# Optimization experiments

Hardware: AMD Instinct MI355X
Metric: run time of the kernel (lower is better)

Reference implementation:

```python
import jax, jax.numpy as jnp
import numpy as np

B, D, K, V, T = 128, 1280, 49, 10000, 40  # batch, hidden, spatial keys, vocab, max words
SOS = 0


def setup_inputs() -> dict:
    key = jax.random.key(0)
    ks = jax.random.split(key, 20)
    s = 0.02
    inp = {
        "img_channels": jax.random.normal(ks[0], (B, D, 7, 7), jnp.float32),
        "pooled": jax.random.normal(ks[1], (B, D), jnp.float32),
        # LSTM (torch order i,f,g,o), stored as [in, 4*hidden]
        "W_ih": jax.random.normal(ks[2], (D, 4 * D), jnp.float32) * s,
        "W_hh": jax.random.normal(ks[3], (D, 4 * D), jnp.float32) * s,
        "b_ih": jnp.zeros((4 * D,), jnp.float32),
        "b_hh": jnp.zeros((4 * D,), jnp.float32),
        # cross-attention: fc_q on hidden (D->D), fc_k/fc_v on spatial (K->K)
        "Wq": jax.random.normal(ks[4], (D, D), jnp.float32) * s,
        "bq": jnp.zeros((D,), jnp.float32),
        "Wk": jax.random.normal(ks[5], (K, K), jnp.float32) * s,
        "bk": jnp.zeros((K,), jnp.float32),
        "Wv": jax.random.normal(ks[6], (K, K), jnp.float32) * s,
        "bv": jnp.zeros((K,), jnp.float32),
        # gating linears (2D -> D)
        "Wh": jax.random.normal(ks[7], (2 * D, D), jnp.float32) * s,
        "bh": jnp.zeros((D,), jnp.float32),
        "Wc": jax.random.normal(ks[8], (2 * D, D), jnp.float32) * s,
        "bc": jnp.zeros((D,), jnp.float32),
        # vocab projection and embedding
        "Wp": jax.random.normal(ks[9], (D, V), jnp.float32) * s,
        "bp": jnp.zeros((V,), jnp.float32),
        "embed": jax.random.normal(ks[10], (V, D), jnp.float32) * s,
    }
    return inp


def _cross_attn(ch, h, Wq, bq, Wk, bk, Wv, bv):
    # ch: [B, D, K]   h: [B, D]
    q = jnp.tanh(h @ Wq + bq)                      # [B, D]
    k = jnp.tanh(ch @ Wk + bk)                     # [B, D, K]
    scores = jnp.einsum('bdk,bd->bk', k, q) / 7.0  # [B, K]
    w = jax.nn.softmax(scores, axis=1)
    v = jnp.tanh(ch @ Wv + bv)                     # [B, D, K]
    return jnp.einsum('bk,bdk->bd', w, v)          # [B, D]


def reference(img_channels, pooled, W_ih, W_hh, b_ih, b_hh,
              Wq, bq, Wk, bk, Wv, bv, Wh, bh, Wc, bc, Wp, bp, embed):
    ch = img_channels.reshape(B, D, K)

    def lstm_cell(x, h, c):
        g = x @ W_ih + b_ih + h @ W_hh + b_hh      # [B, 4D]
        i, f, gg, o = jnp.split(g, 4, axis=-1)
        c_new = jax.nn.sigmoid(f) * c + jax.nn.sigmoid(i) * jnp.tanh(gg)
        h_new = jax.nn.sigmoid(o) * jnp.tanh(c_new)
        return h_new, c_new

    x0 = jnp.broadcast_to(embed[SOS], (B, D))      # start token embedding

    def step(carry, _):
        x, h, c = carry
        h_new, c_new = lstm_cell(x, h, c)
        out = h_new                                # LSTM output, seq_len=1
        # greedy next-token feed (no teacher forcing)
        idx = jnp.argmax(out @ Wp + bp, axis=-1)   # [B]
        x_next = embed[idx]                        # [B, D]
        # attention-gated state update
        ha = _cross_attn(ch, h_new, Wq, bq, Wk, bk, Wv, bv)
        ca = _cross_attn(ch, c_new, Wq, bq, Wk, bk, Wv, bv)
        h2 = jnp.tanh(jnp.concatenate([ha, h_new], -1) @ Wh + bh)
        c2 = jnp.tanh(jnp.concatenate([ca, c_new], -1) @ Wc + bc)
        return (x_next, h2, c2), out

    _, outs = jax.lax.scan(step, (x0, pooled, pooled), None, length=T - 1)
    pred = jnp.concatenate([x0[None], outs], axis=0)   # [T, B, D]
    res = jnp.einsum('tbd,dn->bnt', pred, Wp) + bp[None, :, None]  # [B, V, T]
    return res
```

## Files before the change

kernel.cpp:

```cpp
#include <hip/hip_runtime.h>
#include <hip/hip_fp16.h>

#define NB 128
#define ND 1280
#define NK 49
#define NV 10000
#define NT 40
#define N4D 5120

typedef unsigned long long u64;

__device__ __forceinline__ void gemm_core(
    const float* __restrict__ A0, const float* __restrict__ A1, int asplit, int lda,
    const float* __restrict__ B0, const float* __restrict__ B1, int bsplit, int ldb,
    int n0, int N, int kbase, int kc, float* __restrict__ C)
{
  __shared__ float Al[2][16][132];
  __shared__ float Bl[2][16][68];
  const int tid = threadIdx.x;
  const int tn = tid & 15, tm = tid >> 4;
  float acc[8][4];
#pragma unroll
  for (int i = 0; i < 8; ++i)
#pragma unroll
    for (int j = 0; j < 4; ++j) acc[i][j] = 0.f;

  const int am  = tid >> 1;
  const int ac0 = (tid & 1) * 8;
  const int br  = tid >> 4;
  const int bc  = (tid & 15) * 4;
  const int bcol = n0 + bc;
  const int ntile = kc >> 4;

  float4 ra0, ra1, rb;

  auto load_tile = [&](int t) {
    const int kg = kbase + (t << 4);
    const float* Ab = (kg < asplit) ? (A0 + kg) : (A1 + (kg - asplit));
    const float* Bb = (kg < bsplit) ? (B0 + (size_t)kg * ldb)
                                    : (B1 + (size_t)(kg - bsplit) * ldb);
    ra0 = *(const float4*)(Ab + (size_t)am * lda + ac0);
    ra1 = *(const float4*)(Ab + (size_t)am * lda + ac0 + 4);
    if (bcol < N) rb = *(const float4*)(Bb + (size_t)br * ldb + bcol);
    else rb = make_float4(0.f, 0.f, 0.f, 0.f);
  };
  auto store_tile = [&](int buf) {
    Al[buf][ac0 + 0][am] = ra0.x; Al[buf][ac0 + 1][am] = ra0.y;
    Al[buf][ac0 + 2][am] = ra0.z; Al[buf][ac0 + 3][am] = ra0.w;
    Al[buf][ac0 + 4][am] = ra1.x; Al[buf][ac0 + 5][am] = ra1.y;
    Al[buf][ac0 + 6][am] = ra1.z; Al[buf][ac0 + 7][am] = ra1.w;
    *(float4*)&Bl[buf][br][bc] = rb;
  };

  load_tile(0); store_tile(0); __syncthreads();
  for (int t = 0; t < ntile; ++t) {
    if (t + 1 < ntile) load_tile(t + 1);
    const int buf = t & 1;
#pragma unroll
    for (int kk = 0; kk < 16; ++kk) {
      const float4 a0 = *(const float4*)&Al[buf][kk][tm * 8];
      const float4 a1 = *(const float4*)&Al[buf][kk][tm * 8 + 4];
      const float4 b4 = *(const float4*)&Bl[buf][kk][tn * 4];
      const float amv[8] = {a0.x, a0.y, a0.z, a0.w, a1.x, a1.y, a1.z, a1.w};
      const float bvv[4] = {b4.x, b4.y, b4.z, b4.w};
#pragma unroll
      for (int i = 0; i < 8; ++i)
#pragma unroll
        for (int j = 0; j < 4; ++j)
          acc[i][j] = fmaf(amv[i], bvv[j], acc[i][j]);
    }
    __syncthreads();
    if (t + 1 < ntile) { store_tile((t + 1) & 1); __syncthreads(); }
  }
  const int ccol = n0 + tn * 4;
  if (ccol < N) {
#pragma unroll
    for (int i = 0; i < 8; ++i) {
      float4 v = make_float4(acc[i][0], acc[i][1], acc[i][2], acc[i][3]);
      *(float4*)(C + (size_t)(tm * 8 + i) * N + ccol) = v;
    }
  }
}

__global__ __launch_bounds__(256) void k_gates(const float* __restrict__ x,
    const float* __restrict__ h, const float* __restrict__ Wih,
    const float* __restrict__ Whh, float* __restrict__ part)
{
  int n0 = blockIdx.x * 64, s = blockIdx.y;
  gemm_core(x, h, ND, ND, Wih, Whh, ND, N4D, n0, N4D, s * 320, 320,
            part + (size_t)s * NB * N4D);
}
__global__ __launch_bounds__(256) void k_logits(const float* __restrict__ hn,
    const float* __restrict__ Wp, float* __restrict__ part)
{
  int n0 = blockIdx.x * 64, s = blockIdx.y;
  gemm_core(hn, hn, 1 << 28, ND, Wp, Wp, 1 << 28, NV, n0, NV, s * 320, 320,
            part + (size_t)s * NB * NV);
}
__global__ __launch_bounds__(256) void k_qgemm(const float* __restrict__ hn,
    const float* __restrict__ cn, const float* __restrict__ Wq, float* __restrict__ part)
{
  int n0 = blockIdx.x * 64, s = blockIdx.y, z = blockIdx.z;
  const float* A = z ? cn : hn;
  gemm_core(A, A, 1 << 28, ND, Wq, Wq, 1 << 28, ND, n0, ND, s * 320, 320,
            part + (size_t)s * 256 * ND + (size_t)z * NB * ND);
}
__global__ __launch_bounds__(256) void k_ggemm(const float* __restrict__ att,
    const float* __restrict__ hn, const float* __restrict__ cn,
    const float* __restrict__ Wh, const float* __restrict__ Wc, float* __restrict__ part)
{
  int n0 = blockIdx.x * 64, s = blockIdx.y, z = blockIdx.z;
  const float* A0 = att + (size_t)z * NB * ND;
  const float* A1 = z ? cn : hn;
  const float* Bw = z ? Wc : Wh;
  gemm_core(A0, A1, ND, ND, Bw, Bw, 1 << 28, ND, n0, ND, s * 320, 320,
            part + (size_t)z * 8 * NB * ND + (size_t)s * NB * ND);
}

__global__ __launch_bounds__(256) void k_lstm(const float* __restrict__ part,
    const float* __restrict__ bih, const float* __restrict__ bhh,
    const float* __restrict__ c_st, float* __restrict__ hn, float* __restrict__ cn,
    u64* __restrict__ amax)
{
  int idx = blockIdx.x * 256 + threadIdx.x;
  if (idx < NB) amax[idx] = 0ULL;
  int b = idx / ND, d = idx % ND;
  const float* gp = part + (size_t)b * N4D;
  float gi = bih[d]          + bhh[d];
  float gf = bih[ND + d]     + bhh[ND + d];
  float gg = bih[2 * ND + d] + bhh[2 * ND + d];
  float go = bih[3 * ND + d] + bhh[3 * ND + d];
#pragma unroll
  for (int s = 0; s < 8; ++s) {
    const float* p = gp + (size_t)s * NB * N4D;
    gi += p[d]; gf += p[ND + d]; gg += p[2 * ND + d]; go += p[3 * ND + d];
  }
  float c = c_st[idx];
  float si = 1.f / (1.f + expf(-gi));
  float sf = 1.f / (1.f + expf(-gf));
  float so = 1.f / (1.f + expf(-go));
  float cnew = sf * c + si * tanhf(gg);
  float hnew = so * tanhf(cnew);
  cn[idx] = cnew; hn[idx] = hnew;
}

__device__ __forceinline__ u64 pack_max(float v, int n) {
  unsigned u = __float_as_uint(v);
  u = (u & 0x80000000u) ? ~u : (u | 0x80000000u);
  return ((u64)u << 32) | (u64)(0xFFFFFFFFu - (unsigned)n);
}
__global__ __launch_bounds__(256) void k_lred(const float* __restrict__ part,
    const float* __restrict__ bp, __half* __restrict__ stage, float* __restrict__ outp,
    int tslice, int staged, u64* __restrict__ amax)
{
  int b = blockIdx.y;
  int nbeg = blockIdx.x * 2000, nend = nbeg + 2000;
  u64 best = 0ULL;
  for (int n = nbeg + (int)threadIdx.x; n < nend; n += 256) {
    float v = bp[n];
#pragma unroll
    for (int s = 0; s < 4; ++s) v += part[(size_t)s * NB * NV + (size_t)b * NV + n];
    if (staged) stage[(size_t)tslice * NB * NV + (size_t)b * NV + n] = __float2half(v);
    else outp[((size_t)b * NV + n) * NT + tslice] = v;
    u64 p = pack_max(v, n);
    best = best > p ? best : p;
  }
  __shared__ u64 red[256];
  red[threadIdx.x] = best; __syncthreads();
  for (int off = 128; off > 0; off >>= 1) {
    if ((int)threadIdx.x < off) {
      u64 o = red[threadIdx.x + off];
      if (o > red[threadIdx.x]) red[threadIdx.x] = o;
    }
    __syncthreads();
  }
  if (threadIdx.x == 0) atomicMax(amax + b, red[0]);
}

__global__ __launch_bounds__(256) void k_attn(const float* __restrict__ qpart,
    const float* __restrict__ bq, const float* __restrict__ kmatT,
    const float* __restrict__ vmat, float* __restrict__ att,
    const u64* __restrict__ amax, const float* __restrict__ embed,
    float* __restrict__ x_st)
{
  int bb = blockIdx.x;
  if (bb >= NB) {
    int half = bb - NB;
    for (int idx = half * 81920 + (int)threadIdx.x; idx < (half + 1) * 81920; idx += 256) {
      int b = idx / ND, d = idx % ND;
      int n = (int)(0xFFFFFFFFu - (unsigned)(amax[b] & 0xFFFFFFFFULL));
      x_st[idx] = embed[(size_t)n * ND + d];
    }
    return;
  }
  __shared__ float qh[ND], qc[ND];
  __shared__ float sc[2][64];
  __shared__ float wl[2][64];
  int tid = threadIdx.x;
  for (int d = tid; d < ND; d += 256) {
    float ah = bq[d], ac = bq[d];
#pragma unroll
    for (int s = 0; s < 4; ++s) {
      ah += qpart[(size_t)s * 256 * ND + (size_t)bb * ND + d];
      ac += qpart[(size_t)s * 256 * ND + (size_t)(NB + bb) * ND + d];
    }
    qh[d] = tanhf(ah); qc[d] = tanhf(ac);
  }
  __syncthreads();
  int w = tid >> 6, lane = tid & 63;
  for (int kk = w; kk < NK; kk += 4) {
    const float4* kr = (const float4*)(kmatT + ((size_t)bb * NK + kk) * ND);
    float ah = 0.f, ac = 0.f;
#pragma unroll
    for (int c = 0; c < 5; ++c) {
      float4 kv = kr[c * 64 + lane];
      const float4 q4h = *(const float4*)&qh[(c * 64 + lane) * 4];
      const float4 q4c = *(const float4*)&qc[(c * 64 + lane) * 4];
      ah += kv.x * q4h.x + kv.y * q4h.y + kv.z * q4h.z + kv.w * q4h.w;
      ac += kv.x * q4c.x + kv.y * q4c.y + kv.z * q4c.z + kv.w * q4c.w;
    }
#pragma unroll
    for (int off = 32; off > 0; off >>= 1) {
      ah += __shfl_down(ah, off);
      ac += __shfl_down(ac, off);
    }
    if (lane == 0) { sc[0][kk] = ah / 7.0f; sc[1][kk] = ac / 7.0f; }
  }
  __syncthreads();
  if (w < 2) {
    float s = (lane < NK) ? sc[w][lane] : -3.4e38f;
    float mx = s;
#pragma unroll
    for (int off = 32; off > 0; off >>= 1) mx = fmaxf(mx, __shfl_xor(mx, off));
    float e = (lane < NK) ? expf(s - mx) : 0.f;
    float sum = e;
#pragma unroll
    for (int off = 32; off > 0; off >>= 1) sum += __shfl_xor(sum, off);
    wl[w][lane] = (lane < NK) ? e / sum : 0.f;
  }
  __syncthreads();
  for (int d = tid; d < ND; d += 256) {
    const float4* vr = (const float4*)(vmat + ((size_t)bb * ND + d) * 52);
    float ah = 0.f, ac = 0.f;
#pragma unroll
    for (int c4 = 0; c4 < 13; ++c4) {
      float4 v = vr[c4];
      ah += wl[0][c4 * 4 + 0] * v.x + wl[0][c4 * 4 + 1] * v.y
          + wl[0][c4 * 4 + 2] * v.z + wl[0][c4 * 4 + 3] * v.w;
      ac += wl[1][c4 * 4 + 0] * v.x + wl[1][c4 * 4 + 1] * v.y
          + wl[1][c4 * 4 + 2] * v.z + wl[1][c4 * 4 + 3] * v.w;
    }
    att[(size_t)bb * ND + d] = ah;
    att[(size_t)(NB + bb) * ND + d] = ac;
  }
}

__global__ __launch_bounds__(256) void k_gred(const float* __restrict__ part,
    const float* __restrict__ bh, const float* __restrict__ bc,
    float* __restrict__ h_st, float* __restrict__ c_st)
{
  int idx = blockIdx.x * 256 + threadIdx.x;
  int z = idx / (NB * ND); int rem = idx - z * NB * ND; int d = rem % ND;
  float v = z ? bc[d] : bh[d];
  const float* p = part + (size_t)z * 8 * NB * ND + rem;
#pragma unroll
  for (int s = 0; s < 8; ++s) v += p[(size_t)s * NB * ND];
  v = tanhf(v);
  if (z) c_st[rem] = v; else h_st[rem] = v;
}

__global__ __launch_bounds__(256) void k_init(const float* __restrict__ pooled,
    const float* __restrict__ embed, float* __restrict__ h, float* __restrict__ c,
    float* __restrict__ x)
{
  int idx = blockIdx.x * 256 + threadIdx.x;
  float p = pooled[idx];
  h[idx] = p; c[idx] = p;
  x[idx] = embed[idx % ND];
}

__global__ __launch_bounds__(256) void k_kv(const float* __restrict__ ch,
    const float* __restrict__ Wk, const float* __restrict__ bk,
    const float* __restrict__ Wv, const float* __restrict__ bv,
    float* __restrict__ kmatT, float* __restrict__ vmat)
{
  __shared__ float sbuf[256 * NK];
  __shared__ float Wkl[NK * NK], Wvl[NK * NK], bkl[64], bvl[64];
  int b = blockIdx.y, d0 = blockIdx.x * 256, tid = threadIdx.x;
  for (int i = tid; i < NK * NK; i += 256) { Wkl[i] = Wk[i]; Wvl[i] = Wv[i]; }
  if (tid < NK) { bkl[tid] = bk[tid]; bvl[tid] = bv[tid]; }
  const size_t chbase = ((size_t)b * ND + d0) * NK;
  for (int i = tid; i < 256 * NK; i += 256) sbuf[i] = ch[chbase + i];
  __syncthreads();
  float rr[NK];
#pragma unroll
  for (int k = 0; k < NK; ++k) rr[k] = sbuf[tid * NK + k];
  size_t vb = ((size_t)b * ND + d0 + tid) * 52;
  for (int j = 0; j < NK; ++j) {
    float a = bvl[j];
#pragma unroll
    for (int k = 0; k < NK; ++k) a = fmaf(rr[k], Wvl[k * NK + j], a);
    vmat[vb + j] = tanhf(a);
  }
  vmat[vb + 49] = 0.f; vmat[vb + 50] = 0.f; vmat[vb + 51] = 0.f;
  __syncthreads();
  for (int j = 0; j < NK; ++j) {
    float a = bkl[j];
#pragma unroll
    for (int k = 0; k < NK; ++k) a = fmaf(rr[k], Wkl[k * NK + j], a);
    sbuf[j * 256 + tid] = tanhf(a);
  }
  __syncthreads();
  for (int i = tid; i < NK * 256; i += 256) {
    int j = i >> 8, dd = i & 255;
    kmatT[((size_t)b * NK + j) * ND + d0 + dd] = sbuf[i];
  }
}

__global__ __launch_bounds__(256) void k_l0(const float* __restrict__ embed,
    const float* __restrict__ Wp, const float* __restrict__ bp,
    __half* __restrict__ stage, float* __restrict__ outp, int staged)
{
  __shared__ float e0[ND];
  int tid = threadIdx.x;
  for (int i = tid; i < ND; i += 256) e0[i] = embed[i];
  __syncthreads();
  int n = blockIdx.x * 256 + tid;
  if (n >= NV) return;
  float a = bp[n];
  for (int d = 0; d < ND; ++d) a = fmaf(e0[d], Wp[(size_t)d * NV + n], a);
  if (staged) {
    for (int b = 0; b < NB; ++b) stage[(size_t)b * NV + n] = __float2half(a);
  } else {
    for (int b = 0; b < NB; ++b) outp[((size_t)b * NV + n) * NT] = a;
  }
}

__global__ __launch_bounds__(256) void k_tr(const __half* __restrict__ stage,
    float* __restrict__ outp)
{
  __shared__ float tl[64][41];
  int b = blockIdx.y, n0 = blockIdx.x * 64, tid = threadIdx.x;
  for (int i = tid; i < 2560; i += 256) {
    int t = i >> 6, n = i & 63;
    float v = (n0 + n < NV)
        ? __half2float(stage[(size_t)t * NB * NV + (size_t)b * NV + n0 + n]) : 0.f;
    tl[n][t] = v;
  }
  __syncthreads();
  for (int i = tid; i < 640; i += 256) {
    int row = i / 10, c4 = i % 10;
    if (n0 + row < NV) {
      float4 v = make_float4(tl[row][c4 * 4], tl[row][c4 * 4 + 1],
                             tl[row][c4 * 4 + 2], tl[row][c4 * 4 + 3]);
      *(float4*)(outp + ((size_t)b * NV + n0 + row) * NT + c4 * 4) = v;
    }
  }
}

extern "C" void kernel_launch(void* const* d_in, const int* in_sizes, int n_in,
                              void* d_out, int out_size, void* d_ws, size_t ws_size,
                              hipStream_t stream) {
  const float* ch     = (const float*)d_in[0];
  const float* pooled = (const float*)d_in[1];
  const float* Wih    = (const float*)d_in[2];
  const float* Whh    = (const float*)d_in[3];
  const float* bih    = (const float*)d_in[4];
  const float* bhh    = (const float*)d_in[5];
  const float* Wq     = (const float*)d_in[6];
  const float* bq     = (const float*)d_in[7];
  const float* Wk     = (const float*)d_in[8];
  const float* bk     = (const float*)d_in[9];
  const float* Wv     = (const float*)d_in[10];
  const float* bv     = (const float*)d_in[11];
  const float* Wh     = (const float*)d_in[12];
  const float* bh     = (const float*)d_in[13];
  const float* Wc     = (const float*)d_in[14];
  const float* bc     = (const float*)d_in[15];
  const float* Wp     = (const float*)d_in[16];
  const float* bp     = (const float*)d_in[17];
  const float* embed  = (const float*)d_in[18];
  float* outp = (float*)d_out;

  char* w = (char*)d_ws;
  size_t off = 0;
  auto alloc = [&](size_t bytes) {
    void* p = w + off; off += (bytes + 255) & ~(size_t)255; return p;
  };
  float* kmatT  = (float*)alloc((size_t)NB * NK * ND * 4);
  float* vmat   = (float*)alloc((size_t)NB * ND * 52 * 4);
  float* h_st   = (float*)alloc((size_t)NB * ND * 4);
  float* c_st   = (float*)alloc((size_t)NB * ND * 4);
  float* x_st   = (float*)alloc((size_t)NB * ND * 4);
  float* h_new  = (float*)alloc((size_t)NB * ND * 4);
  float* c_new  = (float*)alloc((size_t)NB * ND * 4);
  float* gpart  = (float*)alloc((size_t)8 * NB * N4D * 4);
  float* lpart  = (float*)alloc((size_t)4 * NB * NV * 4);
  float* qpart  = (float*)alloc((size_t)4 * 256 * ND * 4);
  float* attb   = (float*)alloc((size_t)256 * ND * 4);
  float* g2part = (float*)alloc((size_t)2 * 8 * NB * ND * 4);
  u64*   amax   = (u64*)alloc((size_t)NB * 8);
  __half* stage = (__half*)alloc((size_t)NT * NB * NV * 2);
  int staged = (ws_size >= off) ? 1 : 0;

  k_init<<<640, 256, 0, stream>>>(pooled, embed, h_st, c_st, x_st);
  k_kv<<<dim3(5, NB), 256, 0, stream>>>(ch, Wk, bk, Wv, bv, kmatT, vmat);
  k_l0<<<40, 256, 0, stream>>>(embed, Wp, bp, stage, outp, staged);

  for (int s = 0; s < NT - 1; ++s) {
    k_gates<<<dim3(80, 8), 256, 0, stream>>>(x_st, h_st, Wih, Whh, gpart);
    k_lstm<<<640, 256, 0, stream>>>(gpart, bih, bhh, c_st, h_new, c_new, amax);
    k_logits<<<dim3(157, 4), 256, 0, stream>>>(h_new, Wp, lpart);
    k_lred<<<dim3(5, NB), 256, 0, stream>>>(lpart, bp, stage, outp, s + 1, staged, amax);
    k_qgemm<<<dim3(20, 4, 2), 256, 0, stream>>>(h_new, c_new, Wq, qpart);
    k_attn<<<130, 256, 0, stream>>>(qpart, bq, kmatT, vmat, attb, amax, embed, x_st);
    k_ggemm<<<dim3(20, 8, 2), 256, 0, stream>>>(attb, h_new, c_new, Wh, Wc, g2part);
    k_gred<<<1280, 256, 0, stream>>>(g2part, bh, bc, h_st, c_st);
  }
  if (staged) k_tr<<<dim3(157, NB), 256, 0, stream>>>(stage, outp);
}
```

Measured before the change: 16.63 ms.

## Fuse per-step kernels into persistent cooperative kernel with grid syncs

Replaces eight kernel launches per decode step with one persistent cooperative kernel of 512 blocks that runs the seven phases and separates them with grid-wide barriers. It also changes the split-K partitioning (6, 3, 6 and 12 splits) so each phase fills the fixed grid, and runs the logit reduction concurrently with the Wq GEMM in one phase. The aim is to remove launch overhead and idle tails between many small kernels. In exchange it depends on 512 blocks being co-resident (two per CU), and falls back to per-phase launches if the cooperative launch fails.

```diff
diff --git a/kernel.cpp b/kernel.cpp
--- a/kernel.cpp
+++ b/kernel.cpp
@@ -1,5 +1,8 @@
 #include <hip/hip_runtime.h>
 #include <hip/hip_fp16.h>
+#include <hip/hip_cooperative_groups.h>
+
+namespace cg = cooperative_groups;
 
 #define NB 128
 #define ND 1280
@@ -7,8 +10,20 @@
 #define NV 10000
 #define NT 40
 #define N4D 5120
+#define GRID 512
 
 typedef unsigned long long u64;
+
+struct P {
+  const float *ch, *pooled, *Wih, *Whh, *bih, *bhh, *Wq, *bq, *Wk, *bk, *Wv, *bv,
+              *Wh, *bh, *Wc, *bc, *Wp, *bp, *embed;
+  float *outp;
+  float *kmatT, *vmat, *h_st, *c_st, *x_st, *h_new, *c_new,
+        *gpart, *lpart, *qpart, *attb, *g2part;
+  u64 *amax;
+  __half *stage;
+  int staged;
+};
 
 __device__ __forceinline__ void gemm_core(
     const float* __restrict__ A0, const float* __restrict__ A1, int asplit, int lda,
@@ -82,134 +97,75 @@
   }
 }
 
-__global__ __launch_bounds__(256) void k_gates(const float* __restrict__ x,
-    const float* __restrict__ h, const float* __restrict__ Wih,
-    const float* __restrict__ Whh, float* __restrict__ part)
-{
-  int n0 = blockIdx.x * 64, s = blockIdx.y;
-  gemm_core(x, h, ND, ND, Wih, Whh, ND, N4D, n0, N4D, s * 320, 320,
-            part + (size_t)s * NB * N4D);
-}
-__global__ __launch_bounds__(256) void k_logits(const float* __restrict__ hn,
-    const float* __restrict__ Wp, float* __restrict__ part)
-{
-  int n0 = blockIdx.x * 64, s = blockIdx.y;
-  gemm_core(hn, hn, 1 << 28, ND, Wp, Wp, 1 << 28, NV, n0, NV, s * 320, 320,
-            part + (size_t)s * NB * NV);
-}
-__global__ __launch_bounds__(256) void k_qgemm(const float* __restrict__ hn,
-    const float* __restrict__ cn, const float* __restrict__ Wq, float* __restrict__ part)
-{
-  int n0 = blockIdx.x * 64, s = blockIdx.y, z = blockIdx.z;
-  const float* A = z ? cn : hn;
-  gemm_core(A, A, 1 << 28, ND, Wq, Wq, 1 << 28, ND, n0, ND, s * 320, 320,
-            part + (size_t)s * 256 * ND + (size_t)z * NB * ND);
-}
-__global__ __launch_bounds__(256) void k_ggemm(const float* __restrict__ att,
-    const float* __restrict__ hn, const float* __restrict__ cn,
-    const float* __restrict__ Wh, const float* __restrict__ Wc, float* __restrict__ part)
-{
-  int n0 = blockIdx.x * 64, s = blockIdx.y, z = blockIdx.z;
-  const float* A0 = att + (size_t)z * NB * ND;
-  const float* A1 = z ? cn : hn;
-  const float* Bw = z ? Wc : Wh;
-  gemm_core(A0, A1, ND, ND, Bw, Bw, 1 << 28, ND, n0, ND, s * 320, 320,
-            part + (size_t)z * 8 * NB * ND + (size_t)s * NB * ND);
-}
-
-__global__ __launch_bounds__(256) void k_lstm(const float* __restrict__ part,
-    const float* __restrict__ bih, const float* __restrict__ bhh,
-    const float* __restrict__ c_st, float* __restrict__ hn, float* __restrict__ cn,
-    u64* __restrict__ amax)
-{
-  int idx = blockIdx.x * 256 + threadIdx.x;
-  if (idx < NB) amax[idx] = 0ULL;
-  int b = idx / ND, d = idx % ND;
-  const float* gp = part + (size_t)b * N4D;
-  float gi = bih[d]          + bhh[d];
-  float gf = bih[ND + d]     + bhh[ND + d];
-  float gg = bih[2 * ND + d] + bhh[2 * ND + d];
-  float go = bih[3 * ND + d] + bhh[3 * ND + d];
-#pragma unroll
-  for (int s = 0; s < 8; ++s) {
-    const float* p = gp + (size_t)s * NB * N4D;
-    gi += p[d]; gf += p[ND + d]; gg += p[2 * ND + d]; go += p[3 * ND + d];
-  }
-  float c = c_st[idx];
-  float si = 1.f / (1.f + expf(-gi));
-  float sf = 1.f / (1.f + expf(-gf));
-  float so = 1.f / (1.f + expf(-go));
-  float cnew = sf * c + si * tanhf(gg);
-  float hnew = so * tanhf(cnew);
-  cn[idx] = cnew; hn[idx] = hnew;
-}
-
 __device__ __forceinline__ u64 pack_max(float v, int n) {
   unsigned u = __float_as_uint(v);
   u = (u & 0x80000000u) ? ~u : (u | 0x80000000u);
   return ((u64)u << 32) | (u64)(0xFFFFFFFFu - (unsigned)n);
 }
-__global__ __launch_bounds__(256) void k_lred(const float* __restrict__ part,
-    const float* __restrict__ bp, __half* __restrict__ stage, float* __restrict__ outp,
-    int tslice, int staged, u64* __restrict__ amax)
-{
-  int b = blockIdx.y;
-  int nbeg = blockIdx.x * 2000, nend = nbeg + 2000;
+
+__device__ void ph_lstm(int blk, const P& p) {
+  int tid = threadIdx.x;
+  for (int idx = blk * 256 + tid; idx < NB * ND; idx += GRID * 256) {
+    if (idx < NB) p.amax[idx] = 0ULL;
+    int b = idx / ND, d = idx % ND;
+    const float* gp = p.gpart + (size_t)b * N4D;
+    float gi = p.bih[d]          + p.bhh[d];
+    float gf = p.bih[ND + d]     + p.bhh[ND + d];
+    float gg = p.bih[2 * ND + d] + p.bhh[2 * ND + d];
+    float go = p.bih[3 * ND + d] + p.bhh[3 * ND + d];
+#pragma unroll
+    for (int s = 0; s < 6; ++s) {
+      const float* q = gp + (size_t)s * NB * N4D;
+      gi += q[d]; gf += q[ND + d]; gg += q[2 * ND + d]; go += q[3 * ND + d];
+    }
+    float c = p.c_st[idx];
+    float si = 1.f / (1.f + expf(-gi));
+    float sf = 1.f / (1.f + expf(-gf));
+    float so = 1.f / (1.f + expf(-go));
+    float cnew = sf * c + si * tanhf(gg);
+    p.c_new[idx] = cnew; p.h_new[idx] = so * tanhf(cnew);
+  }
+}
+
+__device__ void ph_lred(int b, int nbeg, int step, const P& p) {
+  __shared__ u64 red[256];
+  int tid = threadIdx.x;
   u64 best = 0ULL;
-  for (int n = nbeg + (int)threadIdx.x; n < nend; n += 256) {
-    float v = bp[n];
-#pragma unroll
-    for (int s = 0; s < 4; ++s) v += part[(size_t)s * NB * NV + (size_t)b * NV + n];
-    if (staged) stage[(size_t)tslice * NB * NV + (size_t)b * NV + n] = __float2half(v);
-    else outp[((size_t)b * NV + n) * NT + tslice] = v;
-    u64 p = pack_max(v, n);
-    best = best > p ? best : p;
-  }
-  __shared__ u64 red[256];
-  red[threadIdx.x] = best; __syncthreads();
+  for (int n = nbeg + tid; n < nbeg + 5000; n += 256) {
+    float v = p.bp[n];
+#pragma unroll
+    for (int s = 0; s < 3; ++s) v += p.lpart[(size_t)s * NB * NV + (size_t)b * NV + n];
+    if (p.staged) p.stage[(size_t)(step + 1) * NB * NV + (size_t)b * NV + n] = __float2half(v);
+    else p.outp[((size_t)b * NV + n) * NT + step + 1] = v;
+    u64 q = pack_max(v, n);
+    best = best > q ? best : q;
+  }
+  red[tid] = best; __syncthreads();
   for (int off = 128; off > 0; off >>= 1) {
-    if ((int)threadIdx.x < off) {
-      u64 o = red[threadIdx.x + off];
-      if (o > red[threadIdx.x]) red[threadIdx.x] = o;
-    }
+    if (tid < off) { u64 o = red[tid + off]; if (o > red[tid]) red[tid] = o; }
     __syncthreads();
   }
-  if (threadIdx.x == 0) atomicMax(amax + b, red[0]);
-}
-
-__global__ __launch_bounds__(256) void k_attn(const float* __restrict__ qpart,
-    const float* __restrict__ bq, const float* __restrict__ kmatT,
-    const float* __restrict__ vmat, float* __restrict__ att,
-    const u64* __restrict__ amax, const float* __restrict__ embed,
-    float* __restrict__ x_st)
-{
-  int bb = blockIdx.x;
-  if (bb >= NB) {
-    int half = bb - NB;
-    for (int idx = half * 81920 + (int)threadIdx.x; idx < (half + 1) * 81920; idx += 256) {
-      int b = idx / ND, d = idx % ND;
-      int n = (int)(0xFFFFFFFFu - (unsigned)(amax[b] & 0xFFFFFFFFULL));
-      x_st[idx] = embed[(size_t)n * ND + d];
-    }
-    return;
-  }
+  if (tid == 0) atomicMax(p.amax + b, red[0]);
+}
+
+__device__ void ph_attn(int bb, const P& p) {
   __shared__ float qh[ND], qc[ND];
   __shared__ float sc[2][64];
   __shared__ float wl[2][64];
   int tid = threadIdx.x;
   for (int d = tid; d < ND; d += 256) {
-    float ah = bq[d], ac = bq[d];
-#pragma unroll
-    for (int s = 0; s < 4; ++s) {
-      ah += qpart[(size_t)s * 256 * ND + (size_t)bb * ND + d];
-      ac += qpart[(size_t)s * 256 * ND + (size_t)(NB + bb) * ND + d];
+    float ah = p.bq[d], ac = p.bq[d];
+#pragma unroll
+    for (int s = 0; s < 6; ++s) {
+      ah += p.qpart[(size_t)s * 256 * ND + (size_t)bb * ND + d];
+      ac += p.qpart[(size_t)s * 256 * ND + (size_t)(NB + bb) * ND + d];
     }
     qh[d] = tanhf(ah); qc[d] = tanhf(ac);
   }
   __syncthreads();
   int w = tid >> 6, lane = tid & 63;
   for (int kk = w; kk < NK; kk += 4) {
-    const float4* kr = (const float4*)(kmatT + ((size_t)bb * NK + kk) * ND);
+    const float4* kr = (const float4*)(p.kmatT + ((size_t)bb * NK + kk) * ND);
     float ah = 0.f, ac = 0.f;
 #pragma unroll
     for (int c = 0; c < 5; ++c) {
@@ -240,7 +196,7 @@
   }
   __syncthreads();
   for (int d = tid; d < ND; d += 256) {
-    const float4* vr = (const float4*)(vmat + ((size_t)bb * ND + d) * 52);
+    const float4* vr = (const float4*)(p.vmat + ((size_t)bb * ND + d) * 52);
     float ah = 0.f, ac = 0.f;
 #pragma unroll
     for (int c4 = 0; c4 < 13; ++c4) {
@@ -250,23 +206,97 @@
       ac += wl[1][c4 * 4 + 0] * v.x + wl[1][c4 * 4 + 1] * v.y
           + wl[1][c4 * 4 + 2] * v.z + wl[1][c4 * 4 + 3] * v.w;
     }
-    att[(size_t)bb * ND + d] = ah;
-    att[(size_t)(NB + bb) * ND + d] = ac;
-  }
-}
-
-__global__ __launch_bounds__(256) void k_gred(const float* __restrict__ part,
-    const float* __restrict__ bh, const float* __restrict__ bc,
-    float* __restrict__ h_st, float* __restrict__ c_st)
-{
-  int idx = blockIdx.x * 256 + threadIdx.x;
-  int z = idx / (NB * ND); int rem = idx - z * NB * ND; int d = rem % ND;
-  float v = z ? bc[d] : bh[d];
-  const float* p = part + (size_t)z * 8 * NB * ND + rem;
-#pragma unroll
-  for (int s = 0; s < 8; ++s) v += p[(size_t)s * NB * ND];
-  v = tanhf(v);
-  if (z) c_st[rem] = v; else h_st[rem] = v;
+    p.attb[(size_t)bb * ND + d] = ah;
+    p.attb[(size_t)(NB + bb) * ND + d] = ac;
+  }
+}
+
+__device__ void do_phase(int phase, int blk, int step, const P& p) {
+  const int tid = threadIdx.x;
+  switch (phase) {
+    case 1:
+      if (blk < 480) {
+        int tile = blk / 6, sk = blk % 6;
+        int kbase = sk * 432, kc = (sk == 5) ? 400 : 432;
+        gemm_core(p.x_st, p.h_st, ND, ND, p.Wih, p.Whh, ND, N4D,
+                  tile * 64, N4D, kbase, kc, p.gpart + (size_t)sk * NB * N4D);
+      }
+      break;
+    case 2: ph_lstm(blk, p); break;
+    case 3:
+      if (blk < 471) {
+        int tile = blk / 3, sk = blk % 3;
+        int kbase = sk * 432, kc = (sk == 2) ? 416 : 432;
+        gemm_core(p.h_new, p.h_new, 1 << 28, ND, p.Wp, p.Wp, 1 << 28, NV,
+                  tile * 64, NV, kbase, kc, p.lpart + (size_t)sk * NB * NV);
+      }
+      break;
+    case 4:
+      if (blk < 256) ph_lred(blk >> 1, (blk & 1) * 5000, step, p);
+      else if (blk >= 272) {
+        int q = blk - 272, z = q / 120, r = q % 120;
+        int tile = r / 6, sk = r % 6;
+        int kbase = sk * 224, kc = (sk == 5) ? 160 : 224;
+        const float* A = z ? p.c_new : p.h_new;
+        gemm_core(A, A, 1 << 28, ND, p.Wq, p.Wq, 1 << 28, ND,
+                  tile * 64, ND, kbase, kc,
+                  p.qpart + (size_t)sk * 256 * ND + (size_t)z * NB * ND);
+      }
+      break;
+    case 5:
+      if (blk < NB) ph_attn(blk, p);
+      else if (blk < 160) {
+        int base = (blk - NB) * 5120;
+        for (int i = base + tid; i < base + 5120; i += 256) {
+          int b = i / ND, d = i % ND;
+          int n = (int)(0xFFFFFFFFu - (unsigned)(p.amax[b] & 0xFFFFFFFFULL));
+          p.x_st[i] = p.embed[(size_t)n * ND + d];
+        }
+      }
+      break;
+    case 6:
+      if (blk < 480) {
+        int z = blk / 240, r = blk % 240;
+        int tile = r / 12, sk = r % 12;
+        int kbase = (sk < 8) ? sk * 224 : 1792 + (sk - 8) * 192;
+        int kc = (sk < 8) ? 224 : 192;
+        const float* A0 = p.attb + (size_t)z * NB * ND;
+        const float* A1 = z ? p.c_new : p.h_new;
+        const float* Bw = z ? p.Wc : p.Wh;
+        gemm_core(A0, A1, ND, ND, Bw, Bw, 1 << 28, ND, tile * 64, ND, kbase, kc,
+                  p.g2part + (size_t)z * 12 * NB * ND + (size_t)sk * NB * ND);
+      }
+      break;
+    case 7:
+      for (int idx = blk * 256 + tid; idx < 2 * NB * ND; idx += GRID * 256) {
+        int z = idx / (NB * ND); int rem = idx - z * NB * ND; int d = rem % ND;
+        float v = z ? p.bc[d] : p.bh[d];
+        const float* q = p.g2part + (size_t)z * 12 * NB * ND + rem;
+#pragma unroll
+        for (int s = 0; s < 12; ++s) v += q[(size_t)s * NB * ND];
+        v = tanhf(v);
+        if (z) p.c_st[rem] = v; else p.h_st[rem] = v;
+      }
+      break;
+  }
+}
+
+__global__ __launch_bounds__(256, 2) void k_loop(P p) {
+  cg::grid_group g = cg::this_grid();
+  const int blk = blockIdx.x;
+  for (int s = 0; s < NT - 1; ++s) {
+    do_phase(1, blk, s, p); g.sync();
+    do_phase(2, blk, s, p); g.sync();
+    do_phase(3, blk, s, p); g.sync();
+    do_phase(4, blk, s, p); g.sync();
+    do_phase(5, blk, s, p); g.sync();
+    do_phase(6, blk, s, p); g.sync();
+    do_phase(7, blk, s, p); g.sync();
+  }
+}
+
+__global__ __launch_bounds__(256, 2) void f_phase(int phase, int step, P p) {
+  do_phase(phase, blockIdx.x, step, p);
 }
 
 __global__ __launch_bounds__(256) void k_init(const float* __restrict__ pooled,
@@ -361,61 +391,62 @@
 extern "C" void kernel_launch(void* const* d_in, const int* in_sizes, int n_in,
                               void* d_out, int out_size, void* d_ws, size_t ws_size,
                               hipStream_t stream) {
-  const float* ch     = (const float*)d_in[0];
-  const float* pooled = (const float*)d_in[1];
-  const float* Wih    = (const float*)d_in[2];
-  const float* Whh    = (const float*)d_in[3];
-  const float* bih    = (const float*)d_in[4];
-  const float* bhh    = (const float*)d_in[5];
-  const float* Wq     = (const float*)d_in[6];
-  const float* bq     = (const float*)d_in[7];
-  const float* Wk     = (const float*)d_in[8];
-  const float* bk     = (const float*)d_in[9];
-  const float* Wv     = (const float*)d_in[10];
-  const float* bv     = (const float*)d_in[11];
-  const float* Wh     = (const float*)d_in[12];
-  const float* bh     = (const float*)d_in[13];
-  const float* Wc     = (const float*)d_in[14];
-  const float* bc     = (const float*)d_in[15];
-  const float* Wp     = (const float*)d_in[16];
-  const float* bp     = (const float*)d_in[17];
-  const float* embed  = (const float*)d_in[18];
-  float* outp = (float*)d_out;
+  P p;
+  p.ch     = (const float*)d_in[0];
+  p.pooled = (const float*)d_in[1];
+  p.Wih    = (const float*)d_in[2];
+  p.Whh    = (const float*)d_in[3];
+  p.bih    = (const float*)d_in[4];
+  p.bhh    = (const float*)d_in[5];
+  p.Wq     = (const float*)d_in[6];
+  p.bq     = (const float*)d_in[7];
+  p.Wk     = (const float*)d_in[8];
+  p.bk     = (const float*)d_in[9];
+  p.Wv     = (const float*)d_in[10];
+  p.bv     = (const float*)d_in[11];
+  p.Wh     = (const float*)d_in[12];
+  p.bh     = (const float*)d_in[13];
+  p.Wc     = (const float*)d_in[14];
+  p.bc     = (const float*)d_in[15];
+  p.Wp     = (const float*)d_in[16];
+  p.bp     = (const float*)d_in[17];
+  p.embed  = (const float*)d_in[18];
+  p.outp   = (float*)d_out;
 
   char* w = (char*)d_ws;
   size_t off = 0;
   auto alloc = [&](size_t bytes) {
-    void* p = w + off; off += (bytes + 255) & ~(size_t)255; return p;
+    void* q = w + off; off += (bytes + 255) & ~(size_t)255; return q;
   };
-  float* kmatT  = (float*)alloc((size_t)NB * NK * ND * 4);
-  float* vmat   = (float*)alloc((size_t)NB * ND * 52 * 4);
-  float* h_st   = (float*)alloc((size_t)NB * ND * 4);
-  float* c_st   = (float*)alloc((size_t)NB * ND * 4);
-  float* x_st   = (float*)alloc((size_t)NB * ND * 4);
-  float* h_new  = (float*)alloc((size_t)NB * ND * 4);
-  float* c_new  = (float*)alloc((size_t)NB * ND * 4);
-  float* gpart  = (float*)alloc((size_t)8 * NB * N4D * 4);
-  float* lpart  = (float*)alloc((size_t)4 * NB * NV * 4);
-  float* qpart  = (float*)alloc((size_t)4 * 256 * ND * 4);
-  float* attb   = (float*)alloc((size_t)256 * ND * 4);
-  float* g2part = (float*)alloc((size_t)2 * 8 * NB * ND * 4);
-  u64*   amax   = (u64*)alloc((size_t)NB * 8);
-  __half* stage = (__half*)alloc((size_t)NT * NB * NV * 2);
-  int staged = (ws_size >= off) ? 1 : 0;
-
-  k_init<<<640, 256, 0, stream>>>(pooled, embed, h_st, c_st, x_st);
-  k_kv<<<dim3(5, NB), 256, 0, stream>>>(ch, Wk, bk, Wv, bv, kmatT, vmat);
-  k_l0<<<40, 256, 0, stream>>>(embed, Wp, bp, stage, outp, staged);
-
-  for (int s = 0; s < NT - 1; ++s) {
-    k_gates<<<dim3(80, 8), 256, 0, stream>>>(x_st, h_st, Wih, Whh, gpart);
-    k_lstm<<<640, 256, 0, stream>>>(gpart, bih, bhh, c_st, h_new, c_new, amax);
-    k_logits<<<dim3(157, 4), 256, 0, stream>>>(h_new, Wp, lpart);
-    k_lred<<<dim3(5, NB), 256, 0, stream>>>(lpart, bp, stage, outp, s + 1, staged, amax);
-    k_qgemm<<<dim3(20, 4, 2), 256, 0, stream>>>(h_new, c_new, Wq, qpart);
-    k_attn<<<130, 256, 0, stream>>>(qpart, bq, kmatT, vmat, attb, amax, embed, x_st);
-    k_ggemm<<<dim3(20, 8, 2), 256, 0, stream>>>(attb, h_new, c_new, Wh, Wc, g2part);
-    k_gred<<<1280, 256, 0, stream>>>(g2part, bh, bc, h_st, c_st);
-  }
-  if (staged) k_tr<<<dim3(157, NB), 256, 0, stream>>>(stage, outp);
-}
+  p.kmatT  = (float*)alloc((size_t)NB * NK * ND * 4);
+  p.vmat   = (float*)alloc((size_t)NB * ND * 52 * 4);
+  p.h_st   = (float*)alloc((size_t)NB * ND * 4);
+  p.c_st   = (float*)alloc((size_t)NB * ND * 4);
+  p.x_st   = (float*)alloc((size_t)NB * ND * 4);
+  p.h_new  = (float*)alloc((size_t)NB * ND * 4);
+  p.c_new  = (float*)alloc((size_t)NB * ND * 4);
+  p.gpart  = (float*)alloc((size_t)6 * NB * N4D * 4);
+  p.lpart  = (float*)alloc((size_t)3 * NB * NV * 4);
+  p.qpart  = (float*)alloc((size_t)6 * 256 * ND * 4);
+  p.attb   = (float*)alloc((size_t)256 * ND * 4);
+  p.g2part = (float*)alloc((size_t)2 * 12 * NB * ND * 4);
+  p.amax   = (u64*)alloc((size_t)NB * 8);
+  p.stage  = (__half*)alloc((size_t)NT * NB * NV * 2);
+  p.staged = (ws_size >= off) ? 1 : 0;
+
+  k_init<<<640, 256, 0, stream>>>(p.pooled, p.embed, p.h_st, p.c_st, p.x_st);
+  k_kv<<<dim3(5, NB), 256, 0, stream>>>(p.ch, p.Wk, p.bk, p.Wv, p.bv, p.kmatT, p.vmat);
+  k_l0<<<40, 256, 0, stream>>>(p.embed, p.Wp, p.bp, p.stage, p.outp, p.staged);
+
+  void* args[] = { &p };
+  hipError_t e = hipLaunchCooperativeKernel((const void*)k_loop, dim3(GRID),
+                                            dim3(256), args, 0, stream);
+  if (e != hipSuccess) {
+    (void)hipGetLastError();
+    for (int s = 0; s < NT - 1; ++s)
+      for (int phase = 1; phase <= 7; ++phase)
+        f_phase<<<GRID, 256, 0, stream>>>(phase, s, p);
+  }
+
+  if (p.staged) k_tr<<<dim3(157, NB), 256, 0, stream>>>(p.stage, p.outp);
+}
```

New measurement: 25.76 ms. +55.0%, slower.
